# Performance work log

Hardware: AMD Instinct MI355X
Metric: run time of the kernel (lower is better)

## Reference

```python
import jax, jax.numpy as jnp
import numpy as np

D_MODEL = 768
NUM_HEADS = 12
D_K = D_MODEL // NUM_HEADS


def setup_inputs() -> dict:
    key = jax.random.key(0)
    ks = jax.random.split(key, 9)
    B, N, C = 32, 577, D_MODEL
    s = 1.0 / np.sqrt(C)
    x = jax.random.normal(ks[0], (B, N, C), dtype=jnp.float32)
    Wq = jax.random.normal(ks[1], (C, C), dtype=jnp.float32) * s
    bq = jnp.zeros((C,), dtype=jnp.float32)
    Wk = jax.random.normal(ks[2], (C, C), dtype=jnp.float32) * s
    bk = jnp.zeros((C,), dtype=jnp.float32)
    Wv = jax.random.normal(ks[3], (C, C), dtype=jnp.float32) * s
    bv = jnp.zeros((C,), dtype=jnp.float32)
    Wo = jax.random.normal(ks[4], (C, C), dtype=jnp.float32) * s
    bo = jnp.zeros((C,), dtype=jnp.float32)
    return {"x": x, "Wq": Wq, "bq": bq, "Wk": Wk, "bk": bk,
            "Wv": Wv, "bv": bv, "Wo": Wo, "bo": bo}


def reference(x, Wq, bq, Wk, bk, Wv, bv, Wo, bo):
    B, N, C = x.shape
    H, dk = NUM_HEADS, D_K
    # Linear projections (torch Linear: x @ W.T + b)
    q = (x @ Wq.T + bq).reshape(B, N, H, dk).transpose(0, 2, 1, 3)  # [B,H,N,dk]
    k = (x @ Wk.T + bk).reshape(B, N, H, dk).transpose(0, 2, 1, 3)
    v = (x @ Wv.T + bv).reshape(B, N, H, dk).transpose(0, 2, 1, 3)
    scale = 1.0 / jnp.sqrt(jnp.asarray(dk, dtype=x.dtype))
    scores = jnp.einsum('bhnd,bhmd->bhnm', q, k) * scale  # [B,H,N,N]
    attn = jax.nn.softmax(scores, axis=-1)
    out = jnp.einsum('bhnm,bhmd->bhnd', attn, v)  # [B,H,N,dk]
    out = out.transpose(0, 2, 1, 3).reshape(B, N, C)
    return out @ Wo.T + bo
```

## Files before the change

kernel.cpp:

```cpp
#include <hip/hip_runtime.h>
#include <cstdint>
#include <cstddef>

typedef float  f32x4   __attribute__((ext_vector_type(4)));
typedef __bf16 bf16x8  __attribute__((ext_vector_type(8)));
typedef short  short8  __attribute__((ext_vector_type(8)));
typedef short  short4v __attribute__((ext_vector_type(4)));
typedef float  float4v __attribute__((ext_vector_type(4)));

#define DEVI __device__ __forceinline__

constexpr int Bb = 32, Nn = 577, Cc = 768, Hh = 12, DK = 64;
constexpr int Mm   = Bb * Nn;
constexpr int NQKV = 3 * Cc;
constexpr int NKPAD = 640;
constexpr int NT = 10;
#define QSCALE 0.1803368926f

DEVI short f2bf(float f) {
  __bf16 h = (__bf16)f;
  short s;
  __builtin_memcpy(&s, &h, 2);
  return s;
}

DEVI float fexp2(float x) { return __builtin_amdgcn_exp2f(x); }

DEVI void gload16(const short* g, short* l) {
  __builtin_amdgcn_global_load_lds(
      (const __attribute__((address_space(1))) void*)g,
      (__attribute__((address_space(3))) void*)l, 16, 0, 0);
}

DEVI f32x4 mfma16(bf16x8 a, bf16x8 b, f32x4 c) {
  return __builtin_amdgcn_mfma_f32_16x16x32_bf16(a, b, c, 0, 0, 0);
}

DEVI void remap_grouped(int bid, int nbm, int nbn, int GM, int& bm, int& bn) {
  const int nwg = nbm * nbn;
  const int xcd = bid & 7, j = bid >> 3;
  const int q = nwg >> 3, r = nwg & 7;
  int wg = (xcd < r ? xcd * (q + 1) : r * (q + 1) + (xcd - r) * q) + j;
  const int per = GM * nbn;
  int grp = wg / per;
  int first = grp * GM;
  int sz = min(GM, nbm - first);
  int rem = wg - grp * per;
  bm = first + rem % sz;
  bn = rem / sz;
}


__global__ void k_cvt_all(const float* __restrict__ x,
                          const float* __restrict__ Wq, const float* __restrict__ Wk,
                          const float* __restrict__ Wv, const float* __restrict__ Wo,
                          short* __restrict__ xb, short* __restrict__ wqkv,
                          short* __restrict__ wob) {
  const int NX4   = Mm * Cc / 4;
  const int WSZ4  = Cc * Cc / 4;
  const int NTOT  = NX4 + 4 * WSZ4;
  for (int i = blockIdx.x * 256 + threadIdx.x; i < NTOT; i += gridDim.x * 256) {
    const float* src;
    short* dst;
    int e;
    if (i < NX4) { src = x; dst = xb; e = i; }
    else {
      int j = i - NX4;
      if (j < WSZ4)          { src = Wq; dst = wqkv;                e = j; }
      else if (j < 2 * WSZ4) { src = Wk; dst = wqkv + WSZ4 * 4;     e = j - WSZ4; }
      else if (j < 3 * WSZ4) { src = Wv; dst = wqkv + 2 * WSZ4 * 4; e = j - 2 * WSZ4; }
      else                   { src = Wo; dst = wob;                 e = j - 3 * WSZ4; }
    }
    float4v v = *(const float4v*)(src + (size_t)e * 4);
    short4v o;
#pragma unroll
    for (int t = 0; t < 4; ++t) o[t] = f2bf(v[t]);
    *(short4v*)(dst + (size_t)e * 4) = o;
  }
}

#define WAITV(N) asm volatile("s_waitcnt vmcnt(" #N ")" ::: "memory")

#define GPH(BUF, KK, MH, STAGE, WAIT)                                      \
  {                                                                        \
    const short* Ab_ = Al + (BUF) * 16384;                                 \
    const short* Bb_ = Bl + (BUF) * 16384;                                 \
    bf16x8 af_[4];                                                         \
    _Pragma("unroll")                                                      \
    for (int m_ = 0; m_ < 4; ++m_)                                         \
      af_[m_] = *(const bf16x8*)(Ab_ + (offA[(MH) * 4 + m_] ^ ((KK) * 32))); \
    if ((MH) == 0) {                                                       \
      _Pragma("unroll")                                                    \
      for (int n_ = 0; n_ < 4; ++n_)                                       \
        bfr[n_] = *(const bf16x8*)(Bb_ + (offB[n_] ^ ((KK) * 32)));        \
    }                                                                      \
    STAGE;                                                                 \
    WAIT;                                                                  \
    __builtin_amdgcn_s_barrier();                                          \
    __builtin_amdgcn_s_setprio(1);                                         \
    _Pragma("unroll")                                                      \
    for (int m_ = 0; m_ < 4; ++m_)                                         \
      _Pragma("unroll")                                                    \
      for (int n_ = 0; n_ < 4; ++n_)                                       \
        acc[(MH) * 4 + m_][n_] = mfma16(af_[m_], bfr[n_], acc[(MH) * 4 + m_][n_]); \
    __builtin_amdgcn_s_setprio(0);                                         \
    __builtin_amdgcn_s_barrier();                                          \
  }

DEVI void gemm256b(const short* __restrict__ A, const short* __restrict__ Bm,
                   int arows, int bm, int bn,
                   short* Al, short* Bl, f32x4 acc[8][4]) {
  const int tid = threadIdx.x;
  const int lane = tid & 63, w = tid >> 6;
  const int wm = w >> 2, wn = w & 3;
  const int qi = lane & 15, g = lane >> 4;

#pragma unroll
  for (int m = 0; m < 8; ++m)
#pragma unroll
    for (int n = 0; n < 4; ++n) acc[m][n] = (f32x4)0.0f;

  const int rloc = tid >> 3, c8 = tid & 7;
  const int gswz = (c8 ^ (rloc & 7)) * 8;
  const short* pA[4];
  const short* pB[4];
#pragma unroll
  for (int s = 0; s < 4; ++s) {
    int ra = bm * 256 + s * 64 + rloc; if (ra > arows - 1) ra = arows - 1;
    pA[s] = A  + (size_t)ra * Cc + gswz;
    pB[s] = Bm + (size_t)(bn * 256 + s * 64 + rloc) * Cc + gswz;
  }
  auto stA = [&](int buf, int s, int co) {
    gload16(pA[s] + co, Al + buf * 16384 + s * 4096 + tid * 8);
  };
  auto stB = [&](int buf, int s, int co) {
    gload16(pB[s] + co, Bl + buf * 16384 + s * 4096 + tid * 8);
  };

  int offA[8], offB[4];
#pragma unroll
  for (int m = 0; m < 8; ++m) {
    int r = wm * 128 + m * 16 + qi;
    offA[m] = r * 64 + ((g ^ (r & 7)) * 8);
  }
#pragma unroll
  for (int n = 0; n < 4; ++n) {
    int r = wn * 64 + n * 16 + qi;
    offB[n] = r * 64 + ((g ^ (r & 7)) * 8);
  }
  bf16x8 bfr[4];

  stA(0, 0, 0); stA(0, 1, 0); stA(0, 2, 0); stA(0, 3, 0);
  stB(0, 0, 0); stB(0, 1, 0); stB(0, 2, 0); stB(0, 3, 0);
  stB(1, 0, 64); stB(1, 1, 64);
  WAITV(2);
  __builtin_amdgcn_s_barrier();

#pragma unroll 1
  for (int i = 0; i < 5; ++i) {
    const int cb1  = 64 + 128 * i;
    const int cb0n = cb1 + 64;
    const int cb1n = cb1 + 128;
    GPH(0, 0, 0, (stB(1, 2, cb1),  stB(1, 3, cb1)),  (void)0);
    GPH(0, 0, 1, (stA(1, 0, cb1),  stA(1, 2, cb1)),  (void)0);
    GPH(0, 1, 0, (stA(1, 1, cb1),  stA(1, 3, cb1)),  (void)0);
    GPH(0, 1, 1, (stA(0, 0, cb0n), stA(0, 2, cb0n)), WAITV(4));
    GPH(1, 0, 0, (stA(0, 1, cb0n), stA(0, 3, cb0n)), WAITV(4));
    GPH(1, 0, 1, (stB(0, 0, cb0n), stB(0, 1, cb0n)), (void)0);
    GPH(1, 1, 0, (stB(0, 2, cb0n), stB(0, 3, cb0n)), (void)0);
    GPH(1, 1, 1, (stB(1, 0, cb1n), stB(1, 1, cb1n)), WAITV(2));
  }
  GPH(0, 0, 0, (stB(1, 2, 704), stB(1, 3, 704)), (void)0);
  GPH(0, 0, 1, (stA(1, 0, 704), stA(1, 2, 704)), (void)0);
  GPH(0, 1, 0, (stA(1, 1, 704), stA(1, 3, 704)), (void)0);
  GPH(0, 1, 1, (void)0, WAITV(2));
  GPH(1, 0, 0, (void)0, WAITV(0));
  GPH(1, 0, 1, (void)0, (void)0);
  GPH(1, 1, 0, (void)0, (void)0);
  GPH(1, 1, 1, (void)0, (void)0);
}

__global__ __launch_bounds__(512) void k_gemm_qkv(
    const short* __restrict__ A, const short* __restrict__ Bm,
    const float* __restrict__ bq, const float* __restrict__ bk, const float* __restrict__ bv,
    short* __restrict__ qv, short* __restrict__ kv, short* __restrict__ vv) {
  __shared__ short Al[2 * 16384];
  __shared__ short Bl[2 * 16384];
  int bm, bn;
  remap_grouped((int)blockIdx.x, (Mm + 255) / 256, NQKV / 256, 4, bm, bn);
  f32x4 acc[8][4];
  gemm256b(A, Bm, Mm, bm, bn, Al, Bl, acc);

  const int lane = threadIdx.x & 63, w = threadIdx.x >> 6;
  const int wm = w >> 2, wn = w & 3;
  const int qi = lane & 15, g = lane >> 4;
  const int cb = bn * 256 + wn * 64;
  const int proj = cb / Cc;
  const int within = cb - proj * Cc;
  const float* bias = proj == 0 ? bq : proj == 1 ? bk : bv;
  short* dst = proj == 0 ? qv : proj == 1 ? kv : vv;
  const float sc = proj == 0 ? QSCALE : 1.0f;
  const int hh = within >> 6;
  float bvv[4];
#pragma unroll
  for (int n = 0; n < 4; ++n) bvv[n] = bias[within + n * 16 + qi];
#pragma unroll
  for (int m = 0; m < 8; ++m)
#pragma unroll
    for (int r = 0; r < 4; ++r) {
      int row = bm * 256 + wm * 128 + m * 16 + g * 4 + r;
      if (row < Mm) {
        int b = row / Nn;
        int nn = row - b * Nn;
        size_t base = ((size_t)(b * Hh + hh) * Nn + nn) * DK;
#pragma unroll
        for (int n = 0; n < 4; ++n)
          dst[base + n * 16 + qi] = f2bf((acc[m][n][r] + bvv[n]) * sc);
      }
    }
}

__global__ __launch_bounds__(512) void k_gemm_out(
    const short* __restrict__ A, const short* __restrict__ Bm,
    const float* __restrict__ bo, float* __restrict__ out) {
  __shared__ short Al[2 * 16384];
  __shared__ short Bl[2 * 16384];
  int bm, bn;
  remap_grouped((int)blockIdx.x, (Mm + 255) / 256, Cc / 256, 8, bm, bn);
  f32x4 acc[8][4];
  gemm256b(A, Bm, Mm, bm, bn, Al, Bl, acc);

  const int lane = threadIdx.x & 63, w = threadIdx.x >> 6;
  const int wm = w >> 2, wn = w & 3;
  const int qi = lane & 15, g = lane >> 4;
  const int cb = bn * 256 + wn * 64;
  float bvv[4];
#pragma unroll
  for (int n = 0; n < 4; ++n) bvv[n] = bo[cb + n * 16 + qi];
#pragma unroll
  for (int m = 0; m < 8; ++m)
#pragma unroll
    for (int r = 0; r < 4; ++r) {
      int row = bm * 256 + wm * 128 + m * 16 + g * 4 + r;
      if (row < Mm) {
#pragma unroll
        for (int n = 0; n < 4; ++n)
          out[(size_t)row * Cc + cb + n * 16 + qi] = acc[m][n][r] + bvv[n];
      }
    }
}

__global__ __launch_bounds__(256) void k_transpose_v(const short* __restrict__ v,
                                                     short* __restrict__ vt) {
  __shared__ short t[64 * 72];
  const int bid = blockIdx.x;
  const int ch = bid % NT, bh = bid / NT;
  const int tid = threadIdx.x;
  const short* vb = v + (size_t)bh * Nn * DK;
#pragma unroll
  for (int i = 0; i < 2; ++i) {
    int gi = i * 256 + tid;
    int r = gi >> 3, c = gi & 7;
    int n = ch * 64 + r;
    short8 val;
#pragma unroll
    for (int j = 0; j < 8; ++j) val[j] = 0;
    if (n < Nn) val = *(const short8*)(vb + (size_t)n * DK + c * 8);
    *(short8*)(t + r * 72 + c * 8) = val;
  }
  __syncthreads();
  short* ob = vt + (size_t)bh * DK * NKPAD + ch * 64;
#pragma unroll
  for (int i = 0; i < 2; ++i) {
    int gi = i * 256 + tid;
    int d = gi >> 3, cg = gi & 7;
    short8 o;
#pragma unroll
    for (int j = 0; j < 8; ++j) o[j] = t[(cg * 8 + j) * 72 + d];
    *(short8*)(ob + (size_t)d * NKPAD + cg * 8) = o;
  }
}

__global__ __launch_bounds__(256) void k_attn(const short* __restrict__ q,
                                              const short* __restrict__ k,
                                              const short* __restrict__ vt,
                                              short* __restrict__ ao) {
  __shared__ short Ks[2][64 * 64];
  __shared__ short Vs[2][64 * 64];
  __shared__ short Ps[4][16 * 64];
  int bid = (int)blockIdx.x;
  bid = (bid & 7) * 240 + (bid >> 3);
  const int qtp = bid % 5, bh = bid / 5;
  const int qt0 = qtp * 2;
  const int bb = bh / Hh, hh = bh - bb * Hh;
  const int tid = threadIdx.x, lane = tid & 63, w = tid >> 6;
  const int qi = lane & 15, g = lane >> 4;

  const short* qb  = q  + (size_t)bh * Nn * DK;
  const short* kb  = k  + (size_t)bh * Nn * DK;
  const short* vtb = vt + (size_t)bh * DK * NKPAD;

  const int qrow = qt0 * 64 + w * 16 + qi;
  const bf16x8 qf0a = *(const bf16x8*)(qb + (size_t)qrow * DK + g * 8);
  const bf16x8 qf1a = *(const bf16x8*)(qb + (size_t)qrow * DK + 32 + g * 8);
  const bf16x8 qf0b = *(const bf16x8*)(qb + (size_t)(qrow + 64) * DK + g * 8);
  const bf16x8 qf1b = *(const bf16x8*)(qb + (size_t)(qrow + 64) * DK + 32 + g * 8);

  const int r0 = tid >> 3, cc = tid & 7;
  const int cs0 = (cc ^ (r0 & 7)) * 8;
  const short* kg = kb + r0 * DK + cs0;
  const short* vg = vtb + (size_t)r0 * NKPAD + cs0;
  short* const Kd0 = &Ks[0][w * 512]; short* const Kd1 = &Ks[1][w * 512];
  short* const Vd0 = &Vs[0][w * 512]; short* const Vd1 = &Vs[1][w * 512];

  auto stage = [&](short* Kd, short* Vd) {
    gload16(kg, Kd);          gload16(kg + 2048,  Kd + 2048);
    gload16(vg, Vd);          gload16(vg + 20480, Vd + 2048);
    kg += 4096;               vg += 64;
  };

  const int swq = qi & 7;
  const short* const KF00 = &Ks[0][qi * 64 + ((g    ) ^ swq) * 8];
  const short* const KF01 = &Ks[0][qi * 64 + ((g + 4) ^ swq) * 8];
  const short* const KF10 = &Ks[1][qi * 64 + ((g    ) ^ swq) * 8];
  const short* const KF11 = &Ks[1][qi * 64 + ((g + 4) ^ swq) * 8];
  const short* const VF00 = &Vs[0][qi * 64 + ((g    ) ^ swq) * 8];
  const short* const VF01 = &Vs[0][qi * 64 + ((g + 4) ^ swq) * 8];
  const short* const VF10 = &Vs[1][qi * 64 + ((g    ) ^ swq) * 8];
  const short* const VF11 = &Vs[1][qi * 64 + ((g + 4) ^ swq) * 8];
  short* const PW0 = &Ps[w][qi * 64 + (((0  + g) ^ (swq << 1)) << 2)];
  short* const PW1 = &Ps[w][qi * 64 + (((4  + g) ^ (swq << 1)) << 2)];
  short* const PW2 = &Ps[w][qi * 64 + (((8  + g) ^ (swq << 1)) << 2)];
  short* const PW3 = &Ps[w][qi * 64 + (((12 + g) ^ (swq << 1)) << 2)];
  const short* const PR0 = &Ps[w][qi * 64 + ((g    ) ^ swq) * 8];
  const short* const PR1 = &Ps[w][qi * 64 + ((g + 4) ^ swq) * 8];

  f32x4 accA[4], accB[4];
#pragma unroll
  for (int nd = 0; nd < 4; ++nd) { accA[nd] = (f32x4)0.0f; accB[nd] = (f32x4)0.0f; }
  float lsA = 0.f, lsB = 0.f;

  auto smax = [&](f32x4* s, float& ls) {
    float rs = 0.f;
    short4v pk0, pk1, pk2, pk3;
#pragma unroll
    for (int r = 0; r < 4; ++r) { float p = fexp2(s[0][r]); rs += p; pk0[r] = f2bf(p); }
#pragma unroll
    for (int r = 0; r < 4; ++r) { float p = fexp2(s[1][r]); rs += p; pk1[r] = f2bf(p); }
#pragma unroll
    for (int r = 0; r < 4; ++r) { float p = fexp2(s[2][r]); rs += p; pk2[r] = f2bf(p); }
#pragma unroll
    for (int r = 0; r < 4; ++r) { float p = fexp2(s[3][r]); rs += p; pk3[r] = f2bf(p); }
    *(short4v*)PW0 = pk0; *(short4v*)PW1 = pk1;
    *(short4v*)PW2 = pk2; *(short4v*)PW3 = pk3;
    rs += __shfl_xor(rs, 16);
    rs += __shfl_xor(rs, 32);
    ls += rs;
  };

  auto tilestep = [&](const short* Kf0, const short* Kf1,
                      const short* Vf0, const short* Vf1) {
    f32x4 sA[4], sB[4];
#pragma unroll
    for (int ni = 0; ni < 4; ++ni) { sA[ni] = (f32x4)0.0f; sB[ni] = (f32x4)0.0f; }
    {
      bf16x8 kf[4];
#pragma unroll
      for (int ni = 0; ni < 4; ++ni) kf[ni] = *(const bf16x8*)(Kf0 + ni * 1024);
#pragma unroll
      for (int ni = 0; ni < 4; ++ni) sA[ni] = mfma16(kf[ni], qf0a, sA[ni]);
#pragma unroll
      for (int ni = 0; ni < 4; ++ni) sB[ni] = mfma16(kf[ni], qf0b, sB[ni]);
#pragma unroll
      for (int ni = 0; ni < 4; ++ni) kf[ni] = *(const bf16x8*)(Kf1 + ni * 1024);
#pragma unroll
      for (int ni = 0; ni < 4; ++ni) sA[ni] = mfma16(kf[ni], qf1a, sA[ni]);
#pragma unroll
      for (int ni = 0; ni < 4; ++ni) sB[ni] = mfma16(kf[ni], qf1b, sB[ni]);
    }
    smax(sA, lsA);
    bf16x8 paA0 = *(const bf16x8*)PR0;
    bf16x8 paA1 = *(const bf16x8*)PR1;
    smax(sB, lsB);
    bf16x8 paB0 = *(const bf16x8*)PR0;
    bf16x8 paB1 = *(const bf16x8*)PR1;
    {
      bf16x8 vf[4];
#pragma unroll
      for (int nd = 0; nd < 4; ++nd) vf[nd] = *(const bf16x8*)(Vf0 + nd * 1024);
#pragma unroll
      for (int nd = 0; nd < 4; ++nd) accA[nd] = mfma16(paA0, vf[nd], accA[nd]);
#pragma unroll
      for (int nd = 0; nd < 4; ++nd) accB[nd] = mfma16(paB0, vf[nd], accB[nd]);
#pragma unroll
      for (int nd = 0; nd < 4; ++nd) vf[nd] = *(const bf16x8*)(Vf1 + nd * 1024);
#pragma unroll
      for (int nd = 0; nd < 4; ++nd) accA[nd] = mfma16(paA1, vf[nd], accA[nd]);
#pragma unroll
      for (int nd = 0; nd < 4; ++nd) accB[nd] = mfma16(paB1, vf[nd], accB[nd]);
    }
  };

  auto lasttile = [&](const short* Kf0, const short* Kf1,
                      const short* Vf0) {
    auto one = [&](const bf16x8& qf0, const bf16x8& qf1, f32x4* accd, float& ls) {
      f32x4 s0 = (f32x4)0.0f;
      s0 = mfma16(*(const bf16x8*)(Kf0), qf0, s0);
      s0 = mfma16(*(const bf16x8*)(Kf1), qf1, s0);
      float rs = 0.f;
      short4v pk0, pkz;
#pragma unroll
      for (int r = 0; r < 4; ++r) {
        float sv = (g == 0 && r == 0) ? s0[r] : -1e30f;
        float p = fexp2(sv);
        rs += p;
        pk0[r] = f2bf(p);
        pkz[r] = 0;
      }
      *(short4v*)PW0 = pk0; *(short4v*)PW1 = pkz;
      rs += __shfl_xor(rs, 16);
      rs += __shfl_xor(rs, 32);
      ls += rs;
      bf16x8 pa0 = *(const bf16x8*)PR0;
#pragma unroll
      for (int nd = 0; nd < 4; ++nd)
        accd[nd] = mfma16(pa0, *(const bf16x8*)(Vf0 + nd * 1024), accd[nd]);
    };
    one(qf0a, qf1a, accA, lsA);
    one(qf0b, qf1b, accB, lsB);
  };

  stage(Kd0, Vd0);
  __syncthreads();
#pragma unroll 1
  for (int t2 = 0; t2 < 5; ++t2) {
    stage(Kd1, Vd1);
    tilestep(KF00, KF01, VF00, VF01);
    __syncthreads();
    if (t2 < 4) {
      stage(Kd0, Vd0);
      tilestep(KF10, KF11, VF10, VF11);
      __syncthreads();
    }
  }
  lasttile(KF10, KF11, VF10);

  auto epi = [&](f32x4* accd, float ls, int qt) {
    float ls4[4];
#pragma unroll
    for (int r = 0; r < 4; ++r) ls4[r] = __shfl(ls, (g << 2) + r);
#pragma unroll
    for (int r = 0; r < 4; ++r) {
      int qr = qt * 64 + w * 16 + (g << 2) + r;
      if (qr < Nn) {
        float inv = 1.0f / ls4[r];
        size_t base = ((size_t)(bb * Nn + qr)) * Cc + hh * DK;
#pragma unroll
        for (int nd = 0; nd < 4; ++nd)
          ao[base + nd * 16 + qi] = f2bf(accd[nd][r] * inv);
      }
    }
  };
  epi(accA, lsA, qt0);
  epi(accB, lsB, qt0 + 1);
}


extern "C" void kernel_launch(void* const* d_in, const int* in_sizes, int n_in,
                              void* d_out, int out_size, void* d_ws, size_t ws_size,
                              hipStream_t stream) {
  const float* x  = (const float*)d_in[0];
  const float* Wq = (const float*)d_in[1];
  const float* bq = (const float*)d_in[2];
  const float* Wk = (const float*)d_in[3];
  const float* bk = (const float*)d_in[4];
  const float* Wv = (const float*)d_in[5];
  const float* bv = (const float*)d_in[6];
  const float* Wo = (const float*)d_in[7];
  const float* bo = (const float*)d_in[8];
  float* out = (float*)d_out;

  char* ws = (char*)d_ws;
  size_t off = 0;
  auto alloc = [&](size_t bytes) {
    char* p = ws + off;
    off += (bytes + 255) & ~(size_t)255;
    return p;
  };
  short* xb   = (short*)alloc((size_t)Mm * Cc * 2);
  short* wqkv = (short*)alloc((size_t)NQKV * Cc * 2);
  short* wob  = (short*)alloc((size_t)Cc * Cc * 2);
  short* qb   = (short*)alloc((size_t)Bb * Hh * Nn * DK * 2);
  short* kb   = (short*)alloc((size_t)Bb * Hh * Nn * DK * 2);
  short* vb   = (short*)alloc((size_t)Bb * Hh * Nn * DK * 2);
  short* vtb  = (short*)alloc((size_t)Bb * Hh * DK * NKPAD * 2);
  short* aob  = xb;

  k_cvt_all<<<4096, 256, 0, stream>>>(x, Wq, Wk, Wv, Wo, xb, wqkv, wob);

  const int nbm = (Mm + 255) / 256;
  k_gemm_qkv<<<nbm * (NQKV / 256), 512, 0, stream>>>(xb, wqkv, bq, bk, bv, qb, kb, vb);

  k_transpose_v<<<Bb * Hh * NT, 256, 0, stream>>>(vb, vtb);

  k_attn<<<Bb * Hh * 5, 256, 0, stream>>>(qb, kb, vtb, aob);

  k_gemm_out<<<nbm * (Cc / 256), 512, 0, stream>>>(aob, wob, bo, out);
}
```

Before: 199.7 us.

## Fuse V transpose into QKV GEMM epilogue via LDS staging

The V-projection tiles of the QKV GEMM now stage their bf16 results in the GEMM's own shared-memory buffers, swizzled so the tile comes out transposed. They then write straight into the transposed, padded V layout that the attention kernel reads. This removes the separate transpose kernel, one launch, and a full write and re-read of the intermediate V tensor. The cost is a heavier epilogue on one third of the GEMM blocks. Risks: shared memory is reused with no explicit barrier after the GEMM main loop, and the padding columns of the transposed V buffer are no longer written with zeros.

```diff
diff --git a/kernel.cpp b/kernel.cpp
--- a/kernel.cpp
+++ b/kernel.cpp
@@ -1,6 +1,7 @@
 #include <hip/hip_runtime.h>
 #include <cstdint>
 #include <cstddef>
+#include <cstring>
 
 typedef float  f32x4   __attribute__((ext_vector_type(4)));
 typedef __bf16 bf16x8  __attribute__((ext_vector_type(8)));
@@ -183,7 +184,7 @@
 __global__ __launch_bounds__(512) void k_gemm_qkv(
     const short* __restrict__ A, const short* __restrict__ Bm,
     const float* __restrict__ bq, const float* __restrict__ bk, const float* __restrict__ bv,
-    short* __restrict__ qv, short* __restrict__ kv, short* __restrict__ vv) {
+    short* __restrict__ qv, short* __restrict__ kv, short* __restrict__ vt) {
   __shared__ short Al[2 * 16384];
   __shared__ short Bl[2 * 16384];
   int bm, bn;
@@ -197,27 +198,69 @@
   const int cb = bn * 256 + wn * 64;
   const int proj = cb / Cc;
   const int within = cb - proj * Cc;
-  const float* bias = proj == 0 ? bq : proj == 1 ? bk : bv;
-  short* dst = proj == 0 ? qv : proj == 1 ? kv : vv;
-  const float sc = proj == 0 ? QSCALE : 1.0f;
   const int hh = within >> 6;
-  float bvv[4];
-#pragma unroll
-  for (int n = 0; n < 4; ++n) bvv[n] = bias[within + n * 16 + qi];
-#pragma unroll
-  for (int m = 0; m < 8; ++m)
-#pragma unroll
-    for (int r = 0; r < 4; ++r) {
-      int row = bm * 256 + wm * 128 + m * 16 + g * 4 + r;
-      if (row < Mm) {
-        int b = row / Nn;
-        int nn = row - b * Nn;
-        size_t base = ((size_t)(b * Hh + hh) * Nn + nn) * DK;
-#pragma unroll
-        for (int n = 0; n < 4; ++n)
-          dst[base + n * 16 + qi] = f2bf((acc[m][n][r] + bvv[n]) * sc);
+
+  if (proj < 2) {
+    const float* bias = proj == 0 ? bq : bk;
+    short* dst = proj == 0 ? qv : kv;
+    const float sc = proj == 0 ? QSCALE : 1.0f;
+    float bvv[4];
+#pragma unroll
+    for (int n = 0; n < 4; ++n) bvv[n] = bias[within + n * 16 + qi];
+#pragma unroll
+    for (int m = 0; m < 8; ++m)
+#pragma unroll
+      for (int r = 0; r < 4; ++r) {
+        int row = bm * 256 + wm * 128 + m * 16 + g * 4 + r;
+        if (row < Mm) {
+          int b = row / Nn;
+          int nn = row - b * Nn;
+          size_t base = ((size_t)(b * Hh + hh) * Nn + nn) * DK;
+#pragma unroll
+          for (int n = 0; n < 4; ++n)
+            dst[base + n * 16 + qi] = f2bf((acc[m][n][r] + bvv[n]) * sc);
+        }
       }
-    }
+  } else {
+    float bvv[4];
+#pragma unroll
+    for (int n = 0; n < 4; ++n) bvv[n] = bv[within + n * 16 + qi];
+    short* sc = (w < 4 ? Al : Bl) + (w & 3) * 8192;
+    const int dq = qi & 7;
+#pragma unroll
+    for (int m = 0; m < 8; ++m)
+#pragma unroll
+      for (int n = 0; n < 4; ++n) {
+        int d = n * 16 + qi;
+        short4v pk;
+#pragma unroll
+        for (int r = 0; r < 4; ++r) pk[r] = f2bf(acc[m][n][r] + bvv[n]);
+        int g8 = 2 * m + (g >> 1);
+        *(short4v*)(sc + d * 128 + ((g8 ^ dq) << 3) + ((g & 1) << 2)) = pk;
+      }
+#pragma unroll
+    for (int it = 0; it < 16; ++it) {
+      int G = it * 64 + lane;
+      int d = G >> 4, cg = G & 15;
+      short8 v = *(const short8*)(sc + d * 128 + ((cg ^ (d & 7)) << 3));
+      int tokg = bm * 256 + wm * 128 + cg * 8;
+      if (tokg < Mm) {
+        int b0 = tokg / Nn, nn0 = tokg - b0 * Nn;
+        if (nn0 + 8 <= Nn) {
+          __builtin_memcpy(vt + ((size_t)(b0 * Hh + hh) * DK + d) * NKPAD + nn0, &v, 16);
+        } else {
+#pragma unroll
+          for (int j = 0; j < 8; ++j) {
+            int tg = tokg + j;
+            if (tg < Mm) {
+              int b1 = tg / Nn, nn1 = tg - b1 * Nn;
+              vt[((size_t)(b1 * Hh + hh) * DK + d) * NKPAD + nn1] = v[j];
+            }
+          }
+        }
+      }
+    }
+  }
 }
 
 __global__ __launch_bounds__(512) void k_gemm_out(
@@ -248,37 +291,6 @@
           out[(size_t)row * Cc + cb + n * 16 + qi] = acc[m][n][r] + bvv[n];
       }
     }
-}
-
-__global__ __launch_bounds__(256) void k_transpose_v(const short* __restrict__ v,
-                                                     short* __restrict__ vt) {
-  __shared__ short t[64 * 72];
-  const int bid = blockIdx.x;
-  const int ch = bid % NT, bh = bid / NT;
-  const int tid = threadIdx.x;
-  const short* vb = v + (size_t)bh * Nn * DK;
-#pragma unroll
-  for (int i = 0; i < 2; ++i) {
-    int gi = i * 256 + tid;
-    int r = gi >> 3, c = gi & 7;
-    int n = ch * 64 + r;
-    short8 val;
-#pragma unroll
-    for (int j = 0; j < 8; ++j) val[j] = 0;
-    if (n < Nn) val = *(const short8*)(vb + (size_t)n * DK + c * 8);
-    *(short8*)(t + r * 72 + c * 8) = val;
-  }
-  __syncthreads();
-  short* ob = vt + (size_t)bh * DK * NKPAD + ch * 64;
-#pragma unroll
-  for (int i = 0; i < 2; ++i) {
-    int gi = i * 256 + tid;
-    int d = gi >> 3, cg = gi & 7;
-    short8 o;
-#pragma unroll
-    for (int j = 0; j < 8; ++j) o[j] = t[(cg * 8 + j) * 72 + d];
-    *(short8*)(ob + (size_t)d * NKPAD + cg * 8) = o;
-  }
 }
 
 __global__ __launch_bounds__(256) void k_attn(const short* __restrict__ q,
@@ -492,16 +504,13 @@
   short* wob  = (short*)alloc((size_t)Cc * Cc * 2);
   short* qb   = (short*)alloc((size_t)Bb * Hh * Nn * DK * 2);
   short* kb   = (short*)alloc((size_t)Bb * Hh * Nn * DK * 2);
-  short* vb   = (short*)alloc((size_t)Bb * Hh * Nn * DK * 2);
   short* vtb  = (short*)alloc((size_t)Bb * Hh * DK * NKPAD * 2);
   short* aob  = xb;
 
   k_cvt_all<<<4096, 256, 0, stream>>>(x, Wq, Wk, Wv, Wo, xb, wqkv, wob);
 
   const int nbm = (Mm + 255) / 256;
-  k_gemm_qkv<<<nbm * (NQKV / 256), 512, 0, stream>>>(xb, wqkv, bq, bk, bv, qb, kb, vb);
-
-  k_transpose_v<<<Bb * Hh * NT, 256, 0, stream>>>(vb, vtb);
+  k_gemm_qkv<<<nbm * (NQKV / 256), 512, 0, stream>>>(xb, wqkv, bq, bk, bv, qb, kb, vtb);
 
   k_attn<<<Bb * Hh * 5, 256, 0, stream>>>(qb, kb, vtb, aob);
 
```

New measurement: 188.2 us (median of 2 runs). -5.8%, faster.
